# Kernel optimization log

Measured on AMD Instinct MI355X. Metric: run time of the kernel, lower is better.

The kernel has to match this reference:

```python
import jax, jax.numpy as jnp
import numpy as np

B, T, C = 2, 2048, 768
H = 12
HD = C // H  # 64
DFF = 4 * C
EPS = 1e-5


def setup_inputs() -> dict:
    key = jax.random.key(0)
    ks = jax.random.split(key, 12)
    s = 0.02
    return {
        "x": jax.random.normal(ks[0], (B, T, C), dtype=jnp.float32),
        "ln1_g": jnp.ones((C,), jnp.float32),
        "ln1_b": jnp.zeros((C,), jnp.float32),
        "w_qkv": jax.random.normal(ks[1], (C, 3 * C), dtype=jnp.float32) * s,
        "w_o": jax.random.normal(ks[2], (C, C), dtype=jnp.float32) * s,
        "ln2_g": jnp.ones((C,), jnp.float32),
        "ln2_b": jnp.zeros((C,), jnp.float32),
        "w_fc": jax.random.normal(ks[3], (C, DFF), dtype=jnp.float32) * s,
        "b_fc": jnp.zeros((DFF,), jnp.float32),
        "w_proj": jax.random.normal(ks[4], (DFF, C), dtype=jnp.float32) * s,
        "b_proj": jnp.zeros((C,), jnp.float32),
    }


def _layernorm(x, g, b):
    mu = jnp.mean(x, axis=-1, keepdims=True)
    var = jnp.mean(jnp.square(x - mu), axis=-1, keepdims=True)
    return (x - mu) * jax.lax.rsqrt(var + EPS) * g + b


def _attn(x, w_qkv, w_o):
    b, t, c = x.shape
    qkv = x @ w_qkv  # [b,t,3c]
    q, k, v = jnp.split(qkv, 3, axis=-1)
    q = q.reshape(b, t, H, HD).transpose(0, 2, 1, 3)  # [b,h,t,d]
    k = k.reshape(b, t, H, HD).transpose(0, 2, 1, 3)
    v = v.reshape(b, t, H, HD).transpose(0, 2, 1, 3)
    att = jnp.einsum("bhqd,bhkd->bhqk", q, k) / jnp.sqrt(jnp.float32(HD))
    causal = jnp.tril(jnp.ones((t, t), dtype=bool))
    att = jnp.where(causal, att, -jnp.inf)
    att = jax.nn.softmax(att, axis=-1)
    y = jnp.einsum("bhqk,bhkd->bhqd", att, v)
    y = y.transpose(0, 2, 1, 3).reshape(b, t, c)
    return y @ w_o


def reference(x, ln1_g, ln1_b, w_qkv, w_o, ln2_g, ln2_b, w_fc, b_fc, w_proj, b_proj):
    x = x + _attn(_layernorm(x, ln1_g, ln1_b), w_qkv, w_o)
    h = _layernorm(x, ln2_g, ln2_b)
    h = jax.nn.gelu(h @ w_fc + b_fc, approximate=False)  # torch F.gelu default = exact erf
    x = x + (h @ w_proj + b_proj)
    return x
```

## Files before the change

kernel.cpp:

```cpp
#include <hip/hip_runtime.h>
#include <hip/hip_bf16.h>
#include <math.h>

#define T_SEQ 2048
#define NB 2
#define C_DIM 768
#define NH 12

typedef unsigned short ushort_t;
typedef __attribute__((ext_vector_type(8))) short short8;
typedef __attribute__((ext_vector_type(8))) unsigned short ushort8;
typedef __attribute__((ext_vector_type(4))) unsigned short ushortx4;
typedef __attribute__((ext_vector_type(4))) float floatx4;
typedef __attribute__((ext_vector_type(4))) _Float16 half4;

__device__ inline float bf2f(ushort_t u) {
    unsigned int x = ((unsigned int)u) << 16;
    return __uint_as_float(x);
}
__device__ inline ushort_t f2bf(float f) {
    unsigned int u = __float_as_uint(f);
    unsigned int r = (u + 0x7fffu + ((u >> 16) & 1u)) >> 16;
    return (ushort_t)r;
}
__device__ inline ushort_t f2h_bits(float f) {
    union { _Float16 h; ushort_t u; } cv;
    cv.h = (_Float16)f;
    return cv.u;
}

#if defined(__has_builtin)
#if __has_builtin(__builtin_amdgcn_global_load_lds)
#define HAVE_GLL 1
#endif
#endif

__device__ inline void gload_lds16(const ushort_t* g, ushort_t* l) {
#ifdef HAVE_GLL
    __builtin_amdgcn_global_load_lds(
        (const __attribute__((address_space(1))) void*)g,
        (__attribute__((address_space(3))) void*)l, 16, 0, 0);
#else
    int lane = threadIdx.x & 63;
    *(ushort8*)(l + lane * 8) = *(const ushort8*)g;
#endif
}

__device__ void wconv_tile(const float* __restrict__ W, ushort_t* __restrict__ WT,
                           int K, int N, int k0, int n0, int tid, ushort_t* Tls) {
    int nl = (tid & 15) * 4;
    int kl = tid >> 4;
#pragma unroll
    for (int rr = 0; rr < 4; rr++) {
        int k = kl + rr * 16;
        floatx4 v = *(const floatx4*)&W[(size_t)(k0 + k) * N + n0 + nl];
#pragma unroll
        for (int j = 0; j < 4; j++) Tls[(nl + j) * 72 + k] = f2bf(v[j]);
    }
    __syncthreads();
    int no = tid >> 3;
    int ko = (tid & 7) * 8;
#pragma unroll
    for (int rr = 0; rr < 2; rr++) {
        int n = no + rr * 32;
        ushort8 t = *(const ushort8*)&Tls[n * 72 + ko];
        *(ushort8*)&WT[(size_t)(n0 + n) * K + k0 + ko] = t;
    }
}

__global__ __launch_bounds__(256) void prep1_kernel(const float* __restrict__ w_qkv, ushort_t* __restrict__ wqkvT,
                                                    const float* __restrict__ w_o, ushort_t* __restrict__ woT,
                                                    const float* __restrict__ w_fc, ushort_t* __restrict__ wfcT,
                                                    const float* __restrict__ w_proj, ushort_t* __restrict__ wprojT,
                                                    const float* __restrict__ x, const float* __restrict__ g,
                                                    const float* __restrict__ b, ushort_t* __restrict__ xn) {
    __shared__ ushort_t Tls[64 * 72];
    __shared__ float red[8];
    int id = blockIdx.x, tid = threadIdx.x;
    if (id < 432) { wconv_tile(w_qkv, wqkvT, 768, 2304, (id % 12) * 64, (id / 12) * 64, tid, Tls); return; }
    if (id < 576) { int r = id - 432; wconv_tile(w_o, woT, 768, 768, (r % 12) * 64, (r / 12) * 64, tid, Tls); return; }
    if (id < 1152) { int r = id - 576; wconv_tile(w_fc, wfcT, 768, 3072, (r % 12) * 64, (r / 12) * 64, tid, Tls); return; }
    if (id < 1728) { int r = id - 1152; wconv_tile(w_proj, wprojT, 3072, 768, (r % 48) * 64, (r / 48) * 64, tid, Tls); return; }
    int row = id - 1728;
    int lane = tid & 63, wave = tid >> 6;
    const float* xr = x + (size_t)row * C_DIM;
    float v0 = xr[tid], v1 = xr[tid + 256], v2 = xr[tid + 512];
    float s = v0 + v1 + v2;
#pragma unroll
    for (int m = 32; m > 0; m >>= 1) s += __shfl_xor(s, m, 64);
    if (lane == 0) red[wave] = s;
    __syncthreads();
    float mean = (red[0] + red[1] + red[2] + red[3]) * (1.0f / C_DIM);
    float d0 = v0 - mean, d1 = v1 - mean, d2 = v2 - mean;
    float q = d0 * d0 + d1 * d1 + d2 * d2;
#pragma unroll
    for (int m = 32; m > 0; m >>= 1) q += __shfl_xor(q, m, 64);
    if (lane == 0) red[wave + 4] = q;
    __syncthreads();
    float var = (red[4] + red[5] + red[6] + red[7]) * (1.0f / C_DIM);
    float rstd = rsqrtf(var + 1e-5f);
    ushort_t* orow = xn + (size_t)row * C_DIM;
    orow[tid]       = f2bf(d0 * rstd * g[tid]       + b[tid]);
    orow[tid + 256] = f2bf(d1 * rstd * g[tid + 256] + b[tid + 256]);
    orow[tid + 512] = f2bf(d2 * rstd * g[tid + 512] + b[tid + 512]);
}

__global__ __launch_bounds__(192) void combine_ln_kernel(const float* __restrict__ x,
                                                         const ushort_t* __restrict__ P,
                                                         const float* __restrict__ g,
                                                         const float* __restrict__ bb,
                                                         float* __restrict__ x2,
                                                         ushort_t* __restrict__ xn) {
    int row = blockIdx.x;
    int tid = threadIdx.x;
    int lane = tid & 63, wave = tid >> 6;
    int col = tid * 4;
    size_t idx = (size_t)row * C_DIM + col;
    floatx4 xv = *(const floatx4*)&x[idx];
    ushortx4 a = *(const ushortx4*)&P[idx];
    ushortx4 b2 = *(const ushortx4*)&P[3145728 + idx];
    ushortx4 c2 = *(const ushortx4*)&P[6291456 + idx];
    floatx4 v;
#pragma unroll
    for (int j = 0; j < 4; j++) v[j] = xv[j] + bf2f(a[j]) + bf2f(b2[j]) + bf2f(c2[j]);
    *(floatx4*)&x2[idx] = v;

    float s = v[0] + v[1] + v[2] + v[3];
#pragma unroll
    for (int m = 32; m > 0; m >>= 1) s += __shfl_xor(s, m, 64);
    __shared__ float red[6];
    if (lane == 0) red[wave] = s;
    __syncthreads();
    float mean = (red[0] + red[1] + red[2]) * (1.0f / C_DIM);
    floatx4 d;
#pragma unroll
    for (int j = 0; j < 4; j++) d[j] = v[j] - mean;
    float q = d[0] * d[0] + d[1] * d[1] + d[2] * d[2] + d[3] * d[3];
#pragma unroll
    for (int m = 32; m > 0; m >>= 1) q += __shfl_xor(q, m, 64);
    if (lane == 0) red[wave + 3] = q;
    __syncthreads();
    float var = (red[3] + red[4] + red[5]) * (1.0f / C_DIM);
    float rstd = rsqrtf(var + 1e-5f);
    floatx4 gv = *(const floatx4*)&g[col];
    floatx4 bv = *(const floatx4*)&bb[col];
    ushortx4 o;
#pragma unroll
    for (int j = 0; j < 4; j++) o[j] = f2bf(d[j] * rstd * gv[j] + bv[j]);
    *(ushortx4*)&xn[idx] = o;
}

#define GEMM_LOOP(Aptr, Bptr, KDIM, KLEN, KOFF)                                        \
    __shared__ ushort_t As[128 * 64];                                                  \
    __shared__ ushort_t Bs[128 * 64];                                                  \
    int tid = threadIdx.x;                                                             \
    int lane = tid & 63, wave = tid >> 6;                                              \
    int lane15 = lane & 15, quad = lane >> 4;                                          \
    int wr = wave >> 1, wc = wave & 1;                                                 \
    int row0 = blockIdx.x * 128, col0 = blockIdx.y * 128;                              \
    int srow = lane >> 3;                                                              \
    int sseg = (lane & 7) ^ srow;                                                      \
    const ushort_t* ag[4]; const ushort_t* bg[4];                                      \
    ushort_t* la[4]; ushort_t* lb[4];                                                  \
    _Pragma("unroll")                                                                  \
    for (int j = 0; j < 4; j++) {                                                      \
        int r = wave * 32 + j * 8;                                                     \
        ag[j] = Aptr + (size_t)(row0 + r + srow) * KDIM + KOFF + sseg * 8;             \
        bg[j] = Bptr + (size_t)(col0 + r + srow) * KDIM + KOFF + sseg * 8;             \
        la[j] = &As[r * 64]; lb[j] = &Bs[r * 64];                                      \
    }                                                                                  \
    floatx4 acc[4][4];                                                                 \
    floatx4 zero = {0.f, 0.f, 0.f, 0.f};                                               \
    _Pragma("unroll")                                                                  \
    for (int mt = 0; mt < 4; mt++)                                                     \
        _Pragma("unroll")                                                              \
        for (int nt = 0; nt < 4; nt++) acc[mt][nt] = zero;                             \
    for (int k0 = 0; k0 < KLEN; k0 += 64) {                                            \
        _Pragma("unroll")                                                              \
        for (int j = 0; j < 4; j++) gload_lds16(ag[j] + k0, la[j]);                    \
        _Pragma("unroll")                                                              \
        for (int j = 0; j < 4; j++) gload_lds16(bg[j] + k0, lb[j]);                    \
        __syncthreads();                                                               \
        _Pragma("unroll")                                                              \
        for (int ko = 0; ko < 2; ko++) {                                               \
            int slot = (quad + ko * 4) ^ (lane15 & 7);                                 \
            short8 af[4], bfm[4];                                                      \
            _Pragma("unroll")                                                          \
            for (int mt = 0; mt < 4; mt++)                                             \
                af[mt] = *(const short8*)&As[(wr * 64 + mt * 16 + lane15) * 64 + slot * 8]; \
            _Pragma("unroll")                                                          \
            for (int nt = 0; nt < 4; nt++)                                             \
                bfm[nt] = *(const short8*)&Bs[(wc * 64 + nt * 16 + lane15) * 64 + slot * 8]; \
            _Pragma("unroll")                                                          \
            for (int mt = 0; mt < 4; mt++)                                             \
                _Pragma("unroll")                                                      \
                for (int nt = 0; nt < 4; nt++)                                         \
                    acc[mt][nt] = __builtin_amdgcn_mfma_f32_16x16x32_bf16(af[mt], bfm[nt], acc[mt][nt], 0, 0, 0); \
        }                                                                              \
        __syncthreads();                                                               \
    }

__global__ __launch_bounds__(256) void gemm_qkv_kernel(const ushort_t* __restrict__ A,
                                                       const ushort_t* __restrict__ BT,
                                                       ushort_t* __restrict__ qbuf,
                                                       ushort_t* __restrict__ kh,
                                                       ushort_t* __restrict__ vtb) {
    GEMM_LOOP(A, BT, 768, 768, 0)
    int yb = blockIdx.y;
    if (yb < 6) {
#pragma unroll
        for (int mt = 0; mt < 4; mt++) {
            int r_base = row0 + wr * 64 + mt * 16 + quad * 4;
#pragma unroll
            for (int nt = 0; nt < 4; nt++) {
                int cc = col0 + wc * 64 + nt * 16 + lane15;
#pragma unroll
                for (int r = 0; r < 4; r++)
                    qbuf[(size_t)(r_base + r) * 768 + cc] = f2bf(acc[mt][nt][r]);
            }
        }
    } else if (yb < 12) {
#pragma unroll
        for (int mt = 0; mt < 4; mt++) {
            int r_base = row0 + wr * 64 + mt * 16 + quad * 4;
#pragma unroll
            for (int nt = 0; nt < 4; nt++) {
                int colk = col0 - 768 + wc * 64 + nt * 16 + lane15;
                int hh = colk >> 6, dd = colk & 63;
#pragma unroll
                for (int r = 0; r < 4; r++) {
                    int rr = r_base + r;
                    kh[((size_t)((rr >> 11) * NH + hh)) * 131072 + (size_t)(rr & 2047) * 64 + dd] =
                        f2bf(acc[mt][nt][r]);
                }
            }
        }
    } else {
#pragma unroll
        for (int mt = 0; mt < 4; mt++) {
            int r_base = row0 + wr * 64 + mt * 16 + quad * 4;
            int bb2 = r_base >> 11;
            int tt = r_base & 2047;
#pragma unroll
            for (int nt = 0; nt < 4; nt++) {
                int colv = col0 - 1536 + wc * 64 + nt * 16 + lane15;
                int hh = colv >> 6, dd = colv & 63;
                size_t va = ((size_t)(bb2 * NH + hh)) * 131072 + (size_t)(tt >> 4) * 1024 +
                            (size_t)dd * 16 + (tt & 15);
                ushortx4 pv;
#pragma unroll
                for (int r = 0; r < 4; r++) pv[r] = f2h_bits(acc[mt][nt][r]);
                *(ushortx4*)&vtb[va] = pv;
            }
        }
    }
}

__global__ __launch_bounds__(256) void gemm_gelu_kernel(const ushort_t* __restrict__ A,
                                                        const ushort_t* __restrict__ BT,
                                                        const float* __restrict__ bias,
                                                        ushort_t* __restrict__ Cout) {
    GEMM_LOOP(A, BT, 768, 768, 0)
    const int N = 3072;
#pragma unroll
    for (int mt = 0; mt < 4; mt++) {
        int r_base = row0 + wr * 64 + mt * 16 + quad * 4;
#pragma unroll
        for (int nt = 0; nt < 4; nt++) {
            int cc = col0 + wc * 64 + nt * 16 + lane15;
            float bvv = bias[cc];
#pragma unroll
            for (int r = 0; r < 4; r++) {
                float v = acc[mt][nt][r] + bvv;
                float y2 = v * (2.3022079f + 0.10294323f * v * v);
                float e = __builtin_amdgcn_exp2f(-y2);
                v = v * __builtin_amdgcn_rcpf(1.f + e);
                Cout[(size_t)(r_base + r) * N + cc] = f2bf(v);
            }
        }
    }
}

__global__ __launch_bounds__(256) void gemm_bt_split_kernel(const ushort_t* __restrict__ A,
                                                            const ushort_t* __restrict__ BT,
                                                            ushort_t* __restrict__ P,
                                                            int M, int N, int K, int klen) {
    int kz0 = blockIdx.z * klen;
    GEMM_LOOP(A, BT, K, klen, kz0)
    ushort_t* Pz = P + (size_t)blockIdx.z * M * N;
#pragma unroll
    for (int mt = 0; mt < 4; mt++) {
        int r_base = row0 + wr * 64 + mt * 16 + quad * 4;
#pragma unroll
        for (int nt = 0; nt < 4; nt++) {
            int cc = col0 + wc * 64 + nt * 16 + lane15;
#pragma unroll
            for (int r = 0; r < 4; r++)
                Pz[(size_t)(r_base + r) * N + cc] = f2bf(acc[mt][nt][r]);
        }
    }
}

__global__ __launch_bounds__(256) void combine_bias_res_kernel(float* __restrict__ x2,
                                                               const float* __restrict__ bias,
                                                               const ushort_t* __restrict__ P) {
    int i = blockIdx.x * 256 + threadIdx.x;
    int col = (i * 4) % C_DIM;
    floatx4 xv = *(const floatx4*)&x2[i * 4];
    floatx4 bv = *(const floatx4*)&bias[col];
    ushortx4 a = *(const ushortx4*)&P[i * 4];
    ushortx4 b = *(const ushortx4*)&P[3145728 + i * 4];
    floatx4 o;
#pragma unroll
    for (int j = 0; j < 4; j++) o[j] = xv[j] + bv[j] + bf2f(a[j]) + bf2f(b[j]);
    *(floatx4*)&x2[i * 4] = o;
}

#define QSCALE 0.18033688f
__global__ __launch_bounds__(256) void attn_kernel(const ushort_t* __restrict__ qbuf,
                                                   const ushort_t* __restrict__ kh,
                                                   const ushort_t* __restrict__ vtb,
                                                   ushort_t* __restrict__ y,
                                                   ushort_t* __restrict__ OP,
                                                   float* __restrict__ LP) {
    __shared__ ushort_t Kb[2][4096];
    __shared__ ushort_t Vb[2][4096];
    int tid = threadIdx.x;
    int lane = tid & 63, wave = tid >> 6;
    int lane15 = lane & 15, quad = lane >> 4;
    int c = blockIdx.x;
    int h = blockIdx.y, b = blockIdx.z;
    int qt, t_start, t_end, half = 0;
    bool is_half;
    if (c < 32) {
        qt = 16 + (c >> 1);
        half = c & 1;
        int ntl = qt + 1, mid = ntl >> 1;
        t_start = half ? mid : 0;
        t_end = half ? ntl : mid;
        is_half = true;
    } else {
        qt = c - 32;
        t_start = 0;
        t_end = qt + 1;
        is_half = false;
    }
    int q0 = qt * 64;
    size_t hb = (size_t)(b * NH + h) * (T_SEQ * 64);
    const ushort_t* khb = kh + hb;
    const ushort_t* vtbb = vtb + hb;

    int q = q0 + wave * 16 + lane15;
    int qmax_wave = q0 + wave * 16 + 15;
    short8 qf[2];
#pragma unroll
    for (int cc2 = 0; cc2 < 2; cc2++) {
        ushort8 qv = *(const ushort8*)(qbuf + ((size_t)b * T_SEQ + q) * 768 + h * 64 + cc2 * 32 + quad * 8);
        short8 qs;
#pragma unroll
        for (int j = 0; j < 8; j++) qs[j] = (short)f2bf(bf2f(qv[j]) * QSCALE);
        qf[cc2] = qs;
    }

    floatx4 o[4];
    floatx4 zero = {0.f, 0.f, 0.f, 0.f};
#pragma unroll
    for (int nt = 0; nt < 4; nt++) o[nt] = zero;
    float l4[4] = {0.f, 0.f, 0.f, 0.f};

    int vsrc = lane ^ ((lane >> 3) & 1);

    {
        int kb = t_start * 64;
        int buf = t_start & 1;
        if (wave < 2) {
#pragma unroll
            for (int j = 0; j < 4; j++) {
                int r = wave * 4 + j;
                int i = r * 64 + lane;
                int key = i >> 3;
                int seg = ((i & 7) - (key & 7) + 8) & 7;
                gload_lds16(khb + (size_t)(kb + key) * 64 + seg * 8, &Kb[buf][(size_t)r * 512]);
            }
        } else {
#pragma unroll
            for (int j = 0; j < 4; j++) {
                int r = (wave - 2) * 4 + j;
                gload_lds16(vtbb + (size_t)(kb >> 4) * 1024 + (size_t)r * 512 + vsrc * 8,
                            &Vb[buf][(size_t)r * 512]);
            }
        }
    }

    for (int t = t_start; t < t_end; t++) {
        int kb = t * 64;
        int cur = t & 1;
        __syncthreads();
        if (t + 1 < t_end) {
            int kb2 = kb + 64;
            int nxt = cur ^ 1;
            if (wave < 2) {
#pragma unroll
                for (int j = 0; j < 4; j++) {
                    int r = wave * 4 + j;
                    int i = r * 64 + lane;
                    int key = i >> 3;
                    int seg = ((i & 7) - (key & 7) + 8) & 7;
                    gload_lds16(khb + (size_t)(kb2 + key) * 64 + seg * 8, &Kb[nxt][(size_t)r * 512]);
                }
            } else {
#pragma unroll
                for (int j = 0; j < 4; j++) {
                    int r = (wave - 2) * 4 + j;
                    gload_lds16(vtbb + (size_t)(kb2 >> 4) * 1024 + (size_t)r * 512 + vsrc * 8,
                                &Vb[nxt][(size_t)r * 512]);
                }
            }
        }

        if (kb <= qmax_wave) {
            const ushort_t* Kc = Kb[cur];
            const _Float16* Vc = (const _Float16*)Vb[cur];

            floatx4 s[4];
#pragma unroll
            for (int sb = 0; sb < 4; sb++) {
                int key = sb * 16 + lane15;
                int s0i = key * 8 + ((quad + key) & 7);
                int s1i = key * 8 + ((quad + 4 + key) & 7);
                short8 kf0 = *(const short8*)(Kc + (size_t)s0i * 8);
                short8 kf1 = *(const short8*)(Kc + (size_t)s1i * 8);
                floatx4 sv = zero;
                sv = __builtin_amdgcn_mfma_f32_16x16x32_bf16(kf0, qf[0], sv, 0, 0, 0);
                sv = __builtin_amdgcn_mfma_f32_16x16x32_bf16(kf1, qf[1], sv, 0, 0, 0);
                s[sb] = sv;
            }

            if (kb + 64 > qmax_wave) {
#pragma unroll
                for (int sb = 0; sb < 4; sb++)
#pragma unroll
                    for (int r = 0; r < 4; r++) {
                        int key = kb + sb * 16 + quad * 4 + r;
                        if (key > q) s[sb][r] = -INFINITY;
                    }
            }

            half4 pf[4];
#pragma unroll
            for (int sb = 0; sb < 4; sb++)
#pragma unroll
                for (int r = 0; r < 4; r++) {
                    float p = __builtin_amdgcn_exp2f(s[sb][r]);
                    l4[r] += p;
                    pf[sb][r] = (_Float16)p;
                }

#pragma unroll
            for (int sb = 0; sb < 4; sb++) {
#pragma unroll
                for (int nt = 0; nt < 4; nt++) {
                    int gg = sb * 128 + (nt * 16 + lane15) * 2 + (quad >> 1);
                    int ss = gg ^ ((gg >> 3) & 1);
                    half4 vf = *(const half4*)&Vc[(size_t)ss * 8 + (quad & 1) * 4];
                    o[nt] = __builtin_amdgcn_mfma_f32_16x16x16f16(vf, pf[sb], o[nt], 0, 0, 0);
                }
            }
        }
    }

    float l_i = (l4[0] + l4[1]) + (l4[2] + l4[3]);
    l_i += __shfl_xor(l_i, 16, 64);
    l_i += __shfl_xor(l_i, 32, 64);

    if (!is_half) {
        float rcp_w = 1.f / l_i;
        ushort_t* yb = y + (size_t)b * T_SEQ * 768;
#pragma unroll
        for (int nt = 0; nt < 4; nt++) {
            ushortx4 st;
#pragma unroll
            for (int r = 0; r < 4; r++) st[r] = f2bf(o[nt][r] * rcp_w);
            *(ushortx4*)&yb[(size_t)q * 768 + h * 64 + nt * 16 + quad * 4] = st;
        }
    } else {
        int tileIdx = (qt - 16) + 16 * (h + NH * b);
        ushort_t* Ob = OP + (size_t)(tileIdx * 2 + half) * 4096;
        float* Lb = LP + (size_t)(tileIdx * 2 + half) * 64;
        if (quad == 0) Lb[wave * 16 + lane15] = l_i;
#pragma unroll
        for (int nt = 0; nt < 4; nt++)
#pragma unroll
            for (int r = 0; r < 4; r++)
                Ob[(nt * 16 + quad * 4 + r) * 64 + wave * 16 + lane15] = f2h_bits(o[nt][r]);
    }
}

__global__ __launch_bounds__(256) void attn_combine_kernel(const ushort_t* __restrict__ OP,
                                                           const float* __restrict__ LP,
                                                           ushort_t* __restrict__ y) {
    int qt = 16 + blockIdx.x;
    int h = blockIdx.y, b = blockIdx.z;
    int tileIdx = blockIdx.x + 16 * (h + NH * b);
    const _Float16* O0 = (const _Float16*)(OP + (size_t)(tileIdx * 2) * 4096);
    const _Float16* O1 = O0 + 4096;
    const float* L0 = LP + (size_t)(tileIdx * 2) * 64;
    const float* L1 = L0 + 64;
    int tid = threadIdx.x;
    ushort_t* yb = y + ((size_t)b * T_SEQ + qt * 64) * 768 + h * 64;
#pragma unroll
    for (int i = 0; i < 16; i++) {
        int idx = tid + i * 256;
        int q = idx >> 6, d = idx & 63;
        float v = (float)O0[d * 64 + q] + (float)O1[d * 64 + q];
        float l = L0[q] + L1[q];
        yb[(size_t)q * 768 + d] = f2bf(v / l);
    }
}

extern "C" void kernel_launch(void* const* d_in, const int* in_sizes, int n_in,
                              void* d_out, int out_size, void* d_ws, size_t ws_size,
                              hipStream_t stream) {
    (void)in_sizes; (void)n_in; (void)out_size; (void)ws_size;
    const float* x      = (const float*)d_in[0];
    const float* ln1_g  = (const float*)d_in[1];
    const float* ln1_b  = (const float*)d_in[2];
    const float* w_qkv  = (const float*)d_in[3];
    const float* w_o    = (const float*)d_in[4];
    const float* ln2_g  = (const float*)d_in[5];
    const float* ln2_b  = (const float*)d_in[6];
    const float* w_fc   = (const float*)d_in[7];
    const float* b_fc   = (const float*)d_in[8];
    const float* w_proj = (const float*)d_in[9];
    const float* b_proj = (const float*)d_in[10];

    char* ws = (char*)d_ws;
    ushort_t* qbuf   = (ushort_t*)(ws);
    ushort_t* kh     = (ushort_t*)(ws + 6291456);
    ushort_t* vtb    = (ushort_t*)(ws + 12582912);
    ushort_t* PA     = (ushort_t*)(ws);
    ushort_t* hff    = (ushort_t*)(ws);
    ushort_t* ybuf   = (ushort_t*)(ws + 18874368);
    ushort_t* xn     = (ushort_t*)(ws + 25165824);
    ushort_t* attnO  = (ushort_t*)(ws + 25165824);
    float*    attnL  = (float*)(ws + 31457280);
    ushort_t* PB     = (ushort_t*)(ws + 25165824);
    ushort_t* wqkvT  = (ushort_t*)(ws + 31457280);
    ushort_t* woT    = (ushort_t*)(ws + 34996224);
    ushort_t* wfcT   = (ushort_t*)(ws + 36175872);
    ushort_t* wprojT = (ushort_t*)(ws + 40894464);
    float* x2 = (float*)d_out;

    const int M = NB * T_SEQ;

    prep1_kernel<<<dim3(5824), 256, 0, stream>>>(w_qkv, wqkvT, w_o, woT, w_fc, wfcT,
                                                 w_proj, wprojT, x, ln1_g, ln1_b, xn);
    gemm_qkv_kernel<<<dim3(32, 18), 256, 0, stream>>>(xn, wqkvT, qbuf, kh, vtb);
    attn_kernel<<<dim3(48, 12, 2), 256, 0, stream>>>(qbuf, kh, vtb, ybuf, attnO, attnL);
    attn_combine_kernel<<<dim3(16, 12, 2), 256, 0, stream>>>(attnO, attnL, ybuf);
    gemm_bt_split_kernel<<<dim3(32, 6, 3), 256, 0, stream>>>(ybuf, woT, PA, M, 768, 768, 256);
    combine_ln_kernel<<<dim3(M), 192, 0, stream>>>(x, PA, ln2_g, ln2_b, x2, xn);
    gemm_gelu_kernel<<<dim3(32, 24), 256, 0, stream>>>(xn, wfcT, b_fc, hff);
    gemm_bt_split_kernel<<<dim3(32, 6, 2), 256, 0, stream>>>(hff, wprojT, PB, M, 768, 3072, 1536);
    combine_bias_res_kernel<<<dim3(3072), 256, 0, stream>>>(x2, b_proj, PB);
}
```

Baseline: 268.9 us.

## Double-buffer GEMM LDS tiles with BK=32 and new swizzle

```diff
diff --git a/kernel.cpp b/kernel.cpp
--- a/kernel.cpp
+++ b/kernel.cpp
@@ -150,54 +150,69 @@
     *(ushortx4*)&xn[idx] = o;
 }
 
-#define GEMM_LOOP(Aptr, Bptr, KDIM, KLEN, KOFF)                                        \
-    __shared__ ushort_t As[128 * 64];                                                  \
-    __shared__ ushort_t Bs[128 * 64];                                                  \
+#define GEMM_LOOP2(Aptr, Bptr, KDIM, KLEN, KOFF)                                       \
+    __shared__ ushort_t As[2][4096];                                                   \
+    __shared__ ushort_t Bs[2][4096];                                                   \
     int tid = threadIdx.x;                                                             \
     int lane = tid & 63, wave = tid >> 6;                                              \
     int lane15 = lane & 15, quad = lane >> 4;                                          \
     int wr = wave >> 1, wc = wave & 1;                                                 \
     int row0 = blockIdx.x * 128, col0 = blockIdx.y * 128;                              \
-    int srow = lane >> 3;                                                              \
-    int sseg = (lane & 7) ^ srow;                                                      \
-    const ushort_t* ag[4]; const ushort_t* bg[4];                                      \
-    ushort_t* la[4]; ushort_t* lb[4];                                                  \
-    _Pragma("unroll")                                                                  \
-    for (int j = 0; j < 4; j++) {                                                      \
-        int r = wave * 32 + j * 8;                                                     \
-        ag[j] = Aptr + (size_t)(row0 + r + srow) * KDIM + KOFF + sseg * 8;             \
-        bg[j] = Bptr + (size_t)(col0 + r + srow) * KDIM + KOFF + sseg * 8;             \
-        la[j] = &As[r * 64]; lb[j] = &Bs[r * 64];                                      \
+    const ushort_t* sp[4];                                                             \
+    ushort_t* dp[2][4];                                                                \
+    {                                                                                  \
+        bool sA = (wave < 2);                                                          \
+        int cw = sA ? wave : (wave - 2);                                               \
+        const ushort_t* Mp = sA ? (Aptr) : (Bptr);                                     \
+        int rb = sA ? row0 : col0;                                                     \
+        _Pragma("unroll")                                                              \
+        for (int j = 0; j < 4; j++) {                                                  \
+            int c = cw * 4 + j;                                                        \
+            int g = c * 64 + lane;                                                     \
+            int row = g >> 2, j2 = g & 3;                                              \
+            int s = (j2 - (row >> 1)) & 3;                                             \
+            sp[j] = Mp + (size_t)(rb + row) * (KDIM) + (KOFF) + s * 8;                 \
+            dp[0][j] = sA ? &As[0][c * 512] : &Bs[0][c * 512];                         \
+            dp[1][j] = sA ? &As[1][c * 512] : &Bs[1][c * 512];                         \
+        }                                                                              \
     }                                                                                  \
     floatx4 acc[4][4];                                                                 \
-    floatx4 zero = {0.f, 0.f, 0.f, 0.f};                                               \
+    {                                                                                  \
+        floatx4 zz = {0.f, 0.f, 0.f, 0.f};                                             \
+        _Pragma("unroll")                                                              \
+        for (int mt = 0; mt < 4; mt++)                                                 \
+            _Pragma("unroll")                                                          \
+            for (int nt = 0; nt < 4; nt++) acc[mt][nt] = zz;                           \
+    }                                                                                  \
     _Pragma("unroll")                                                                  \
-    for (int mt = 0; mt < 4; mt++)                                                     \
+    for (int j = 0; j < 4; j++) gload_lds16(sp[j], dp[0][j]);                          \
+    int n_tiles = (KLEN) / 32;                                                         \
+    for (int t = 0; t < n_tiles; t++) {                                                \
+        int cur = t & 1;                                                               \
+        __syncthreads();                                                               \
+        if (t + 1 < n_tiles) {                                                         \
+            _Pragma("unroll")                                                          \
+            for (int j = 0; j < 4; j++)                                                \
+                gload_lds16(sp[j] + (t + 1) * 32, dp[cur ^ 1][j]);                     \
+        }                                                                              \
+        const ushort_t* Ac = As[cur];                                                  \
+        const ushort_t* Bc = Bs[cur];                                                  \
+        short8 af[4], bfm[4];                                                          \
         _Pragma("unroll")                                                              \
-        for (int nt = 0; nt < 4; nt++) acc[mt][nt] = zero;                             \
-    for (int k0 = 0; k0 < KLEN; k0 += 64) {                                            \
+        for (int mt = 0; mt < 4; mt++) {                                               \
+            int ra = wr * 64 + mt * 16 + lane15;                                       \
+            af[mt] = *(const short8*)&Ac[ra * 32 + (((quad + (ra >> 1)) & 3) << 3)];   \
+        }                                                                              \
         _Pragma("unroll")                                                              \
-        for (int j = 0; j < 4; j++) gload_lds16(ag[j] + k0, la[j]);                    \
+        for (int nt = 0; nt < 4; nt++) {                                               \
+            int rb2 = wc * 64 + nt * 16 + lane15;                                      \
+            bfm[nt] = *(const short8*)&Bc[rb2 * 32 + (((quad + (rb2 >> 1)) & 3) << 3)];\
+        }                                                                              \
         _Pragma("unroll")                                                              \
-        for (int j = 0; j < 4; j++) gload_lds16(bg[j] + k0, lb[j]);                    \
-        __syncthreads();                                                               \
-        _Pragma("unroll")                                                              \
-        for (int ko = 0; ko < 2; ko++) {                                               \
-            int slot = (quad + ko * 4) ^ (lane15 & 7);                                 \
-            short8 af[4], bfm[4];                                                      \
-            _Pragma("unroll")                                                          \
-            for (int mt = 0; mt < 4; mt++)                                             \
-                af[mt] = *(const short8*)&As[(wr * 64 + mt * 16 + lane15) * 64 + slot * 8]; \
+        for (int mt = 0; mt < 4; mt++)                                                 \
             _Pragma("unroll")                                                          \
             for (int nt = 0; nt < 4; nt++)                                             \
-                bfm[nt] = *(const short8*)&Bs[(wc * 64 + nt * 16 + lane15) * 64 + slot * 8]; \
-            _Pragma("unroll")                                                          \
-            for (int mt = 0; mt < 4; mt++)                                             \
-                _Pragma("unroll")                                                      \
-                for (int nt = 0; nt < 4; nt++)                                         \
-                    acc[mt][nt] = __builtin_amdgcn_mfma_f32_16x16x32_bf16(af[mt], bfm[nt], acc[mt][nt], 0, 0, 0); \
-        }                                                                              \
-        __syncthreads();                                                               \
+                acc[mt][nt] = __builtin_amdgcn_mfma_f32_16x16x32_bf16(af[mt], bfm[nt], acc[mt][nt], 0, 0, 0); \
     }
 
 __global__ __launch_bounds__(256) void gemm_qkv_kernel(const ushort_t* __restrict__ A,
@@ -205,7 +220,7 @@
                                                        ushort_t* __restrict__ qbuf,
                                                        ushort_t* __restrict__ kh,
                                                        ushort_t* __restrict__ vtb) {
-    GEMM_LOOP(A, BT, 768, 768, 0)
+    GEMM_LOOP2(A, BT, 768, 768, 0)
     int yb = blockIdx.y;
     if (yb < 6) {
 #pragma unroll
@@ -260,7 +275,7 @@
                                                         const ushort_t* __restrict__ BT,
                                                         const float* __restrict__ bias,
                                                         ushort_t* __restrict__ Cout) {
-    GEMM_LOOP(A, BT, 768, 768, 0)
+    GEMM_LOOP2(A, BT, 768, 768, 0)
     const int N = 3072;
 #pragma unroll
     for (int mt = 0; mt < 4; mt++) {
@@ -286,7 +301,7 @@
                                                             ushort_t* __restrict__ P,
                                                             int M, int N, int K, int klen) {
     int kz0 = blockIdx.z * klen;
-    GEMM_LOOP(A, BT, K, klen, kz0)
+    GEMM_LOOP2(A, BT, K, klen, kz0)
     ushort_t* Pz = P + (size_t)blockIdx.z * M * N;
 #pragma unroll
     for (int mt = 0; mt < 4; mt++) {
```

Measured after the change: 266.0 us. About the same (-1.1%).
